# Performance work log

Hardware: AMD Instinct MI355X
Metric: run time of the kernel (lower is better)

## Reference

```python
import jax, jax.numpy as jnp
import numpy as np
from jax import lax

N = 500_000          # num voxels
LATENT = 128         # latent_dim
DESC = 32            # descriptor_dim
G = 128              # voxel grid side
B = 2                # batches
K = 256              # max centers (hardcoded topk in module)
TAU = 0.1
MIN_SCORE = 0.5
R = 1                # peak_radius
BASE = G + 2         # padded hash base so stencil offsets never collide
NEG = -1e30

# radius_graph with r = R + 0.1 on integer coords -> exact stencil offsets
_OFFS = [(dx, dy, dz)
         for dx in range(-R, R + 1)
         for dy in range(-R, R + 1)
         for dz in range(-R, R + 1)
         if dx * dx + dy * dy + dz * dz <= (R + 0.1) ** 2]
DKEYS = np.array([dx * BASE * BASE + dy * BASE + dz for dx, dy, dz in _OFFS], np.int32)  # (7,)


def setup_inputs() -> dict:
    rng = np.random.default_rng(0)
    lin = rng.choice(B * G ** 3, size=N, replace=False)  # unique occupied voxels
    b = lin // G ** 3
    rem = lin % G ** 3
    coords = np.stack([b, rem // (G * G), (rem // G) % G, rem % G], 1).astype(np.int32)
    key = jax.random.key(0)
    k1, k2, k3, k4, k5, k6, k7 = jax.random.split(key, 7)
    s = 1.0 / np.sqrt(LATENT)
    return {
        "coords": jnp.asarray(coords),
        "voxel_feats": jax.random.normal(k1, (N, LATENT), jnp.float32),
        "centroid_scores": jax.random.uniform(k2, (N, 1), jnp.float32),
        "Wv": jax.random.normal(k3, (LATENT, DESC), jnp.float32) * s,
        "bv": jax.random.normal(k4, (DESC,), jnp.float32) * 0.01,
        "Wc": jax.random.normal(k5, (LATENT, DESC), jnp.float32) * s,
        "bc": jax.random.normal(k6, (DESC,), jnp.float32) * 0.01,
        "bg": jax.random.normal(k7, (DESC,), jnp.float32) * 0.02,
    }


def _find_centroid_peaks(coords, voxel_feats, centroid_scores):
    """Replicates _find_centroid_peaks with fixed K=256 padding (torch.no_grad block)."""
    n = coords.shape[0]
    scores = centroid_scores[:, 0]
    mask = scores > TAU
    # hash each voxel; +1 padding so stencil neighbors never wrap across rows/batches
    keyv = (coords[:, 0] * BASE + coords[:, 1] + 1) * BASE * BASE \
         + (coords[:, 2] + 1) * BASE + (coords[:, 3] + 1)
    order = jnp.argsort(keyv)
    keys_s = keyv[order]
    ms = jnp.where(mask, scores, NEG)  # only masked points participate in the graph

    nk = keyv[:, None] + jnp.asarray(DKEYS)[None, :]          # (N,7) neighbor keys
    pos = jnp.clip(jnp.searchsorted(keys_s, nk.ravel()), 0, n - 1).reshape(n, len(DKEYS))
    found = keys_s[pos] == nk                                  # (N,7) geometric hit
    j = order[pos]                                             # (N,7) neighbor index
    found = found & mask[j] & mask[:, None]                    # edges need both masked

    neigh_max = jnp.max(jnp.where(found, ms[j], NEG), axis=1)  # scatter_max over edges
    peak_mask = mask & (scores >= neigh_max - 1e-6) & (scores >= MIN_SCORE)

    # topk-256 peaks (padded with NEG if fewer)
    vals, top_idx = lax.top_k(jnp.where(peak_mask, scores, NEG), K)
    valid_peak = vals > NEG / 2
    owner_init = jnp.full((n,), -1, jnp.int32).at[top_idx].set(
        jnp.where(valid_peak, jnp.arange(K, dtype=jnp.int32), -1))

    # ownership propagation: a voxel is owned by a neighboring (top) peak; self-loop
    # keeps peaks owning themselves. Conflicts resolved by max (torch scatter is
    # nondeterministic here).
    owner = jnp.max(jnp.where(found, owner_init[j], -1), axis=1)
    owner = jnp.where(mask, owner, -1)

    valid = owner >= 0
    owner_safe = jnp.where(valid, owner, 0)
    sums = jax.ops.segment_sum(jnp.where(valid[:, None], voxel_feats, 0.0),
                               owner_safe, num_segments=K)
    counts = jax.ops.segment_sum(valid.astype(jnp.float32), owner_safe, num_segments=K)
    feat_mean = sums / jnp.maximum(counts, 1.0)[:, None]       # scatter_mean
    conf = jnp.where(valid_peak, vals, 0.0)[:, None]           # (K,1)
    return conf, feat_mean


def reference(coords, voxel_feats, centroid_scores, Wv, bv, Wc, bc, bg):
    conf, feat_mean = _find_centroid_peaks(coords, voxel_feats, centroid_scores)
    conf = lax.stop_gradient(conf)
    feat_mean = lax.stop_gradient(feat_mean)
    voxel_desc = voxel_feats @ Wv + bv              # 1x1 sparse conv == linear
    center_desc = feat_mean @ Wc + bc               # 1x1 sparse conv == linear
    cols = jnp.concatenate([bg[None, :], conf * center_desc], axis=0)  # (K+1, DESC)
    instance_output = voxel_desc @ cols.T            # (N, K+1)
    return conf, instance_output
```

## Files before the change

kernel.cpp:

```cpp
#include <hip/hip_runtime.h>
#include <hip/hip_bf16.h>
#include <stdint.h>

#define TAUF 0.1f
#define MIN_SCOREF 0.5f
#define KTOP 256
#define BASE 130
#define BASE2 16900
#define TABLE_N 4394000
#define NEGF (-1e30f)
#define CAP2 3072
#define NS 4096

__global__ void k_build(const int* __restrict__ coords, int* __restrict__ table,
                        int* __restrict__ keys, int n) {
  int i = blockIdx.x * 256 + threadIdx.x;
  if (i >= n) return;
  int4 c = ((const int4*)coords)[i];
  int key = (c.x * BASE + c.y + 1) * BASE2 + (c.z + 1) * BASE + (c.w + 1);
  keys[i] = key;
  table[key] = i;
}

__global__ void k_peak(const float* __restrict__ scores, const int* __restrict__ keys,
                       const int* __restrict__ table, uint2* __restrict__ cand,
                       int* __restrict__ cand_cnt, int n) {
  int i = blockIdx.x * 256 + threadIdx.x;
  if (i >= n) return;
  float s = scores[i];
  if (!(s > TAUF)) return;
  int key = keys[i];
  const int dk[7] = {-BASE2, -BASE, -1, 0, 1, BASE, BASE2};
  float nm = NEGF;
#pragma unroll
  for (int o = 0; o < 7; ++o) {
    int j = table[key + dk[o]];
    if (j >= 0) {
      float sj = scores[j];
      if (sj > TAUF) nm = fmaxf(nm, sj);
    }
  }
  if (s >= nm - 1e-6f && s >= MIN_SCOREF) {
    int p = atomicAdd(cand_cnt, 1);
    if (p < n) cand[p] = make_uint2(__float_as_uint(s), (unsigned)i);
  }
}

__global__ void k_select(const uint2* __restrict__ cand, const int* __restrict__ cand_cnt,
                         float* __restrict__ conf_out, int* __restrict__ owner_init,
                         int* __restrict__ peak_vox) {
  __shared__ int hist[2048];
  __shared__ unsigned long long keys_s[NS];
  __shared__ int bstar_s, m_s;
  int t = threadIdx.x;
  int nc = *cand_cnt;
  for (int b = t; b < 2048; b += 1024) hist[b] = 0;
  if (t == 0) m_s = 0;
  __syncthreads();
  for (int idx = t; idx < nc; idx += 1024) {
    unsigned sb = cand[idx].x;
    int b = (int)((sb - 0x3F000000u) >> 12);
    b = min(max(b, 0), 2047);
    atomicAdd(&hist[b], 1);
  }
  __syncthreads();
  if (t == 0) {
    int target = min(nc, KTOP);
    int run = 0, bs = 0;
    for (int b = 2047; b >= 0; --b) {
      run += hist[b];
      if (run >= target) { bs = b; break; }
    }
    bstar_s = bs;
  }
  __syncthreads();
  int bs = bstar_s;
  for (int idx = t; idx < nc; idx += 1024) {
    uint2 cv = cand[idx];
    int b = (int)((cv.x - 0x3F000000u) >> 12);
    b = min(max(b, 0), 2047);
    if (b >= bs) {
      int p = atomicAdd(&m_s, 1);
      if (p < CAP2)
        keys_s[p] = ((unsigned long long)cv.x << 32) | (unsigned)(~cv.y);
    }
  }
  __syncthreads();
  int m = min(m_s, CAP2);
  for (int idx = t; idx < NS; idx += 1024)
    if (idx >= m) keys_s[idx] = 0ULL;
  __syncthreads();
  for (int k2 = 2; k2 <= NS; k2 <<= 1) {
    for (int j2 = k2 >> 1; j2 > 0; j2 >>= 1) {
      for (int i = t; i < NS; i += 1024) {
        int ixj = i ^ j2;
        if (ixj > i) {
          unsigned long long a = keys_s[i], b = keys_s[ixj];
          bool descSeg = ((i & k2) == 0);
          bool sw = descSeg ? (a < b) : (a > b);
          if (sw) { keys_s[i] = b; keys_s[ixj] = a; }
        }
      }
      __syncthreads();
    }
  }
  if (t < KTOP) {
    int navail = min(nc, KTOP);
    if (t < navail) {
      unsigned long long kk = keys_s[t];
      float sc = __uint_as_float((unsigned)(kk >> 32));
      int vi = (int)(~(unsigned)(kk & 0xFFFFFFFFu));
      conf_out[t] = sc;
      owner_init[vi] = t;
      peak_vox[t] = vi;
    } else {
      conf_out[t] = 0.0f;
      peak_vox[t] = -1;
    }
  }
}

__global__ void k_owner(const float* __restrict__ scores, const int* __restrict__ keys,
                        const int* __restrict__ table, const int* __restrict__ owner_init,
                        const int* __restrict__ peak_vox, int* __restrict__ visited,
                        const float* __restrict__ feats, float* __restrict__ sums,
                        float* __restrict__ counts) {
  int t = blockIdx.x * blockDim.x + threadIdx.x;
  if (t >= KTOP * 7) return;
  int p = t / 7, o = t % 7;
  int v0 = peak_vox[p];
  if (v0 < 0) return;
  const int dk[7] = {-BASE2, -BASE, -1, 0, 1, BASE, BASE2};
  int v = table[keys[v0] + dk[o]];
  if (v < 0) return;
  if (!(scores[v] > TAUF)) return;
  int kv = keys[v];
  int own = -1;
#pragma unroll
  for (int oo = 0; oo < 7; ++oo) {
    int j = table[kv + dk[oo]];
    if (j >= 0 && scores[j] > TAUF) own = max(own, owner_init[j]);
  }
  if (own < 0) return;
  if (atomicCAS(&visited[v], 0, 1) == 0) {
    atomicAdd(&counts[own], 1.0f);
    const float* fv = feats + (size_t)v * 128;
    float* so = sums + own * 128;
    for (int d = 0; d < 128; ++d) atomicAdd(&so[d], fv[d]);
  }
}

__global__ void k_cols(const float* __restrict__ sums, const float* __restrict__ counts,
                       const float* __restrict__ conf, const float* __restrict__ Wc,
                       const float* __restrict__ bc, const float* __restrict__ bg,
                       float* __restrict__ colsT) {
  int gid = blockIdx.x * blockDim.x + threadIdx.x;
  if (gid >= 32 * 257) return;
  int kd = gid / 257, jo = gid % 257;
  float val;
  if (jo == 0) {
    val = bg[kd];
  } else {
    int p = jo - 1;
    float inv = 1.0f / fmaxf(counts[p], 1.0f);
    float acc = bc[kd];
    const float* sp = sums + p * 128;
    for (int c = 0; c < 128; ++c) acc += sp[c] * inv * Wc[c * 32 + kd];
    val = conf[p] * acc;
  }
  colsT[kd * 257 + jo] = val;
}

__global__ __launch_bounds__(256) void k_desc(const float* __restrict__ feats,
                                              const float* __restrict__ Wv,
                                              const float* __restrict__ bv,
                                              float* __restrict__ desc, int n) {
  __shared__ __align__(16) float Wv_s[128 * 32];
  __shared__ float feats_s[64 * 129];
  __shared__ float bv_s[32];
  int t = threadIdx.x;
  int rbase = blockIdx.x * 64;
  {
    const float4* src = (const float4*)Wv;
    float4* dst = (float4*)Wv_s;
    for (int i = t; i < 1024; i += 256) dst[i] = src[i];
  }
  if (t < 32) bv_s[t] = bv[t];
  for (int it = 0; it < 8; ++it) {
    int idx = t + it * 256;
    int r = idx >> 5, c4 = idx & 31;
    int row = rbase + r;
    float4 v = make_float4(0.f, 0.f, 0.f, 0.f);
    if (row < n) v = *(const float4*)(feats + (size_t)row * 128 + c4 * 4);
    float* fd = &feats_s[r * 129 + c4 * 4];
    fd[0] = v.x; fd[1] = v.y; fd[2] = v.z; fd[3] = v.w;
  }
  __syncthreads();
  int r = t & 63;
  int k0 = (t >> 6) * 8;
  float acc[8];
#pragma unroll
  for (int q = 0; q < 8; ++q) acc[q] = bv_s[k0 + q];
  const float* fr = &feats_s[r * 129];
#pragma unroll 8
  for (int c = 0; c < 128; ++c) {
    float f = fr[c];
    float4 w0 = *(const float4*)&Wv_s[c * 32 + k0];
    float4 w1 = *(const float4*)&Wv_s[c * 32 + k0 + 4];
    acc[0] += f * w0.x; acc[1] += f * w0.y; acc[2] += f * w0.z; acc[3] += f * w0.w;
    acc[4] += f * w1.x; acc[5] += f * w1.y; acc[6] += f * w1.z; acc[7] += f * w1.w;
  }
  int row = rbase + r;
  if (row < n) {
    float4* dp = (float4*)(desc + (size_t)row * 32 + k0);
    dp[0] = make_float4(acc[0], acc[1], acc[2], acc[3]);
    dp[1] = make_float4(acc[4], acc[5], acc[6], acc[7]);
  }
}

__global__ __launch_bounds__(256) void k_out(const float* __restrict__ desc,
                                             const float* __restrict__ colsT,
                                             float* __restrict__ out, int n) {
  __shared__ __align__(16) float cols_s[32 * 260];
  __shared__ float desc_s[192 * 33];
  int t = threadIdx.x;
  int rbase = blockIdx.x * 192;
  for (int idx = t; idx < 32 * 257; idx += 256) {
    int kd = idx / 257, jo = idx % 257;
    cols_s[kd * 260 + jo] = colsT[idx];
  }
  for (int it = 0; it < 6; ++it) {
    int idx = t + it * 256;
    int r = idx >> 3, c4 = idx & 7;
    int row = rbase + r;
    float4 v = make_float4(0.f, 0.f, 0.f, 0.f);
    if (row < n) v = *(const float4*)(desc + (size_t)row * 32 + c4 * 4);
    float* dd = &desc_s[r * 33 + c4 * 4];
    dd[0] = v.x; dd[1] = v.y; dd[2] = v.z; dd[3] = v.w;
  }
  __syncthreads();
  int jg = t & 7, rg = t >> 3;
  int r0 = rg * 6;
  for (int jc = 0; jc < 4; ++jc) {
    int j0 = jc * 64 + jg * 8;
    float acc[6][8];
#pragma unroll
    for (int a = 0; a < 6; ++a)
#pragma unroll
      for (int b = 0; b < 8; ++b) acc[a][b] = 0.f;
#pragma unroll 4
    for (int k = 0; k < 32; ++k) {
      float4 c0 = *(const float4*)&cols_s[k * 260 + j0];
      float4 c1 = *(const float4*)&cols_s[k * 260 + j0 + 4];
      float cj[8] = {c0.x, c0.y, c0.z, c0.w, c1.x, c1.y, c1.z, c1.w};
#pragma unroll
      for (int rr = 0; rr < 6; ++rr) {
        float f = desc_s[(r0 + rr) * 33 + k];
#pragma unroll
        for (int jj = 0; jj < 8; ++jj) acc[rr][jj] += f * cj[jj];
      }
    }
#pragma unroll
    for (int rr = 0; rr < 6; ++rr) {
      int row = rbase + r0 + rr;
      if (row < n) {
        float* op = out + 256 + (size_t)row * 257 + j0;
#pragma unroll
        for (int jj = 0; jj < 8; ++jj) op[jj] = acc[rr][jj];
      }
    }
  }
  if (t < 192) {
    float accT = 0.f;
#pragma unroll 8
    for (int k = 0; k < 32; ++k) accT += desc_s[t * 33 + k] * cols_s[k * 260 + 256];
    int row = rbase + t;
    if (row < n) out[256 + (size_t)row * 257 + 256] = accT;
  }
}

__global__ void k_M(const float* __restrict__ Wv, const float* __restrict__ bv,
                    const float* __restrict__ colsT, float* __restrict__ M) {
  int gid = blockIdx.x * 256 + threadIdx.x;
  if (gid >= 129 * 257) return;
  int c = gid / 257, jo = gid % 257;
  const float* wrow = (c < 128) ? (Wv + c * 32) : bv;
  float acc = 0.f;
  for (int k = 0; k < 32; ++k) acc += wrow[k] * colsT[k * 257 + jo];
  M[gid] = acc;
}
__global__ void k_fused(const float* __restrict__ feats, const float* __restrict__ M,
                        float* __restrict__ out, int n) {
  long long gid = (long long)blockIdx.x * 256 + threadIdx.x;
  if (gid >= (long long)n * 257) return;
  int i = (int)(gid / 257), jo = (int)(gid % 257);
  const float* fr = feats + (size_t)i * 128;
  float acc = M[128 * 257 + jo];
  for (int c = 0; c < 128; ++c) acc += fr[c] * M[c * 257 + jo];
  out[256 + gid] = acc;
}

extern "C" void kernel_launch(void* const* d_in, const int* in_sizes, int n_in,
                              void* d_out, int out_size, void* d_ws, size_t ws_size,
                              hipStream_t stream) {
  const int*   coords = (const int*)d_in[0];
  const float* feats  = (const float*)d_in[1];
  const float* scores = (const float*)d_in[2];
  const float* Wv     = (const float*)d_in[3];
  const float* bv     = (const float*)d_in[4];
  const float* Wc     = (const float*)d_in[5];
  const float* bc     = (const float*)d_in[6];
  const float* bg     = (const float*)d_in[7];
  float* out = (float*)d_out;
  int n = in_sizes[0] / 4;

  char* ws = (char*)d_ws;
  size_t off = 0;
  auto alloc = [&](size_t bytes) -> char* {
    char* p = ws + off;
    off = (off + bytes + 255) & ~(size_t)255;
    return p;
  };
  int*   table      = (int*)alloc((size_t)TABLE_N * 4);
  int*   keys       = (int*)alloc((size_t)n * 4);
  int*   owner_init = (int*)alloc((size_t)n * 4);
  char*  zero_base  = ws + off;
  int*   visited    = (int*)alloc((size_t)n * 4);
  int*   cand_cnt   = (int*)alloc(256);
  float* sums       = (float*)alloc(256 * 128 * 4);
  float* counts     = (float*)alloc(256 * 4);
  size_t zero_bytes = (size_t)((ws + off) - zero_base);
  uint2* cand       = (uint2*)alloc((size_t)n * 8);
  int*   peak_vox   = (int*)alloc(KTOP * 4);
  float* colsT      = (float*)alloc(32 * 257 * 4);
  size_t off_common = off;
  float* desc       = (float*)alloc((size_t)n * 32 * 4);
  bool use_split = (off <= ws_size);

  hipMemsetAsync(table, 0xFF, (size_t)TABLE_N * 4, stream);
  hipMemsetAsync(owner_init, 0xFF, (size_t)n * 4, stream);
  hipMemsetAsync(zero_base, 0, zero_bytes, stream);

  int nb = (n + 255) / 256;
  k_build<<<nb, 256, 0, stream>>>(coords, table, keys, n);
  k_peak<<<nb, 256, 0, stream>>>(scores, keys, table, cand, cand_cnt, n);
  k_select<<<1, 1024, 0, stream>>>(cand, cand_cnt, out, owner_init, peak_vox);
  k_owner<<<7, 256, 0, stream>>>(scores, keys, table, owner_init, peak_vox,
                                 visited, feats, sums, counts);
  k_cols<<<(32 * 257 + 255) / 256, 256, 0, stream>>>(sums, counts, out, Wc, bc, bg, colsT);

  if (use_split) {
    k_desc<<<(n + 63) / 64, 256, 0, stream>>>(feats, Wv, bv, desc, n);
    k_out<<<(n + 191) / 192, 256, 0, stream>>>(desc, colsT, out, n);
  } else {
    off = off_common;
    float* M = (float*)alloc(129 * 257 * 4);
    k_M<<<(129 * 257 + 255) / 256, 256, 0, stream>>>(Wv, bv, colsT, M);
    long long total = (long long)n * 257;
    int nbf = (int)((total + 255) / 256);
    k_fused<<<nbf, 256, 0, stream>>>(feats, M, out, n);
  }
}
```

Baseline: 1.194 ms.

## Fuse descriptor and output GEMMs, build histogram in peak kernel, shrink sort

The voxel-descriptor GEMM and the output GEMM are merged into one kernel that processes 192 rows per block in chunks of 32. This removes the round trip of the N×32 descriptor buffer through global memory. The score histogram is now built with global atomics inside the peak kernel, and the selection kernel uses a two-level prefix scan. The bitonic sort is sized to the next power of two at or above the candidate count instead of a fixed 4096. The two memsets are merged into one by placing table and owner_init next to each other. The fused kernel uses more shared memory and has less register reuse per output (one row per thread group instead of six), which may lower GEMM efficiency.

```diff
diff --git a/kernel.cpp b/kernel.cpp
--- a/kernel.cpp
+++ b/kernel.cpp
@@ -1,5 +1,4 @@
 #include <hip/hip_runtime.h>
-#include <hip/hip_bf16.h>
 #include <stdint.h>
 
 #define TAUF 0.1f
@@ -10,7 +9,9 @@
 #define TABLE_N 4394000
 #define NEGF (-1e30f)
 #define CAP2 3072
-#define NS 4096
+#define NSMAX 4096
+#define ROWS_PB 192
+#define CHUNK 32
 
 __global__ void k_build(const int* __restrict__ coords, int* __restrict__ table,
                         int* __restrict__ keys, int n) {
@@ -24,7 +25,7 @@
 
 __global__ void k_peak(const float* __restrict__ scores, const int* __restrict__ keys,
                        const int* __restrict__ table, uint2* __restrict__ cand,
-                       int* __restrict__ cand_cnt, int n) {
+                       int* __restrict__ cand_cnt, int* __restrict__ hist, int n) {
   int i = blockIdx.x * 256 + threadIdx.x;
   if (i >= n) return;
   float s = scores[i];
@@ -43,33 +44,51 @@
   if (s >= nm - 1e-6f && s >= MIN_SCOREF) {
     int p = atomicAdd(cand_cnt, 1);
     if (p < n) cand[p] = make_uint2(__float_as_uint(s), (unsigned)i);
-  }
-}
-
-__global__ void k_select(const uint2* __restrict__ cand, const int* __restrict__ cand_cnt,
-                         float* __restrict__ conf_out, int* __restrict__ owner_init,
-                         int* __restrict__ peak_vox) {
-  __shared__ int hist[2048];
-  __shared__ unsigned long long keys_s[NS];
+    unsigned sb = __float_as_uint(s);
+    int b = (int)((sb - 0x3F000000u) >> 12);
+    b = min(max(b, 0), 2047);
+    atomicAdd(&hist[b], 1);
+  }
+}
+
+__global__ __launch_bounds__(1024) void k_select(const uint2* __restrict__ cand,
+                                                 const int* __restrict__ cand_cnt,
+                                                 const int* __restrict__ hist,
+                                                 float* __restrict__ conf_out,
+                                                 int* __restrict__ owner_init,
+                                                 int* __restrict__ peak_vox) {
+  __shared__ int hist_s[2048];
+  __shared__ int part[64];
+  __shared__ unsigned long long keys_s[NSMAX];
   __shared__ int bstar_s, m_s;
   int t = threadIdx.x;
   int nc = *cand_cnt;
-  for (int b = t; b < 2048; b += 1024) hist[b] = 0;
+  for (int b = t; b < 2048; b += 1024) hist_s[b] = hist[b];
   if (t == 0) m_s = 0;
   __syncthreads();
-  for (int idx = t; idx < nc; idx += 1024) {
-    unsigned sb = cand[idx].x;
-    int b = (int)((sb - 0x3F000000u) >> 12);
-    b = min(max(b, 0), 2047);
-    atomicAdd(&hist[b], 1);
+  if (t < 64) {
+    int acc = 0;
+    for (int b = t * 32; b < t * 32 + 32; ++b) acc += hist_s[b];
+    part[t] = acc;
   }
   __syncthreads();
   if (t == 0) {
     int target = min(nc, KTOP);
-    int run = 0, bs = 0;
-    for (int b = 2047; b >= 0; --b) {
-      run += hist[b];
-      if (run >= target) { bs = b; break; }
+    int bs = 0;
+    if (target > 0) {
+      int run = 0, w = 63;
+      for (; w >= 0; --w) {
+        if (run + part[w] >= target) break;
+        run += part[w];
+      }
+      if (w < 0) {
+        bs = 0;
+      } else {
+        for (int b = w * 32 + 31;; --b) {
+          run += hist_s[b];
+          if (run >= target || b == w * 32) { bs = b; break; }
+        }
+      }
     }
     bstar_s = bs;
   }
@@ -87,12 +106,14 @@
   }
   __syncthreads();
   int m = min(m_s, CAP2);
-  for (int idx = t; idx < NS; idx += 1024)
+  int ns = 256;
+  while (ns < m) ns <<= 1;
+  for (int idx = t; idx < ns; idx += 1024)
     if (idx >= m) keys_s[idx] = 0ULL;
   __syncthreads();
-  for (int k2 = 2; k2 <= NS; k2 <<= 1) {
+  for (int k2 = 2; k2 <= ns; k2 <<= 1) {
     for (int j2 = k2 >> 1; j2 > 0; j2 >>= 1) {
-      for (int i = t; i < NS; i += 1024) {
+      for (int i = t; i < ns; i += 1024) {
         int ixj = i ^ j2;
         if (ixj > i) {
           unsigned long long a = keys_s[i], b = keys_s[ixj];
@@ -171,133 +192,90 @@
   colsT[kd * 257 + jo] = val;
 }
 
-__global__ __launch_bounds__(256) void k_desc(const float* __restrict__ feats,
-                                              const float* __restrict__ Wv,
-                                              const float* __restrict__ bv,
-                                              float* __restrict__ desc, int n) {
+__global__ __launch_bounds__(256) void k_go(const float* __restrict__ feats,
+                                            const float* __restrict__ Wv,
+                                            const float* __restrict__ bv,
+                                            const float* __restrict__ colsT,
+                                            float* __restrict__ out, int n) {
   __shared__ __align__(16) float Wv_s[128 * 32];
-  __shared__ float feats_s[64 * 129];
+  __shared__ __align__(16) float cols_s[32 * 260];
+  __shared__ __align__(16) float feats_s[CHUNK * 129];
+  __shared__ float desc_s[CHUNK * 33];
   __shared__ float bv_s[32];
   int t = threadIdx.x;
-  int rbase = blockIdx.x * 64;
+  int rbase = blockIdx.x * ROWS_PB;
   {
     const float4* src = (const float4*)Wv;
     float4* dst = (float4*)Wv_s;
     for (int i = t; i < 1024; i += 256) dst[i] = src[i];
   }
-  if (t < 32) bv_s[t] = bv[t];
-  for (int it = 0; it < 8; ++it) {
-    int idx = t + it * 256;
-    int r = idx >> 5, c4 = idx & 31;
-    int row = rbase + r;
-    float4 v = make_float4(0.f, 0.f, 0.f, 0.f);
-    if (row < n) v = *(const float4*)(feats + (size_t)row * 128 + c4 * 4);
-    float* fd = &feats_s[r * 129 + c4 * 4];
-    fd[0] = v.x; fd[1] = v.y; fd[2] = v.z; fd[3] = v.w;
-  }
-  __syncthreads();
-  int r = t & 63;
-  int k0 = (t >> 6) * 8;
-  float acc[8];
-#pragma unroll
-  for (int q = 0; q < 8; ++q) acc[q] = bv_s[k0 + q];
-  const float* fr = &feats_s[r * 129];
-#pragma unroll 8
-  for (int c = 0; c < 128; ++c) {
-    float f = fr[c];
-    float4 w0 = *(const float4*)&Wv_s[c * 32 + k0];
-    float4 w1 = *(const float4*)&Wv_s[c * 32 + k0 + 4];
-    acc[0] += f * w0.x; acc[1] += f * w0.y; acc[2] += f * w0.z; acc[3] += f * w0.w;
-    acc[4] += f * w1.x; acc[5] += f * w1.y; acc[6] += f * w1.z; acc[7] += f * w1.w;
-  }
-  int row = rbase + r;
-  if (row < n) {
-    float4* dp = (float4*)(desc + (size_t)row * 32 + k0);
-    dp[0] = make_float4(acc[0], acc[1], acc[2], acc[3]);
-    dp[1] = make_float4(acc[4], acc[5], acc[6], acc[7]);
-  }
-}
-
-__global__ __launch_bounds__(256) void k_out(const float* __restrict__ desc,
-                                             const float* __restrict__ colsT,
-                                             float* __restrict__ out, int n) {
-  __shared__ __align__(16) float cols_s[32 * 260];
-  __shared__ float desc_s[192 * 33];
-  int t = threadIdx.x;
-  int rbase = blockIdx.x * 192;
   for (int idx = t; idx < 32 * 257; idx += 256) {
     int kd = idx / 257, jo = idx % 257;
     cols_s[kd * 260 + jo] = colsT[idx];
   }
-  for (int it = 0; it < 6; ++it) {
-    int idx = t + it * 256;
-    int r = idx >> 3, c4 = idx & 7;
-    int row = rbase + r;
-    float4 v = make_float4(0.f, 0.f, 0.f, 0.f);
-    if (row < n) v = *(const float4*)(desc + (size_t)row * 32 + c4 * 4);
-    float* dd = &desc_s[r * 33 + c4 * 4];
-    dd[0] = v.x; dd[1] = v.y; dd[2] = v.z; dd[3] = v.w;
-  }
-  __syncthreads();
-  int jg = t & 7, rg = t >> 3;
-  int r0 = rg * 6;
-  for (int jc = 0; jc < 4; ++jc) {
-    int j0 = jc * 64 + jg * 8;
-    float acc[6][8];
-#pragma unroll
-    for (int a = 0; a < 6; ++a)
-#pragma unroll
-      for (int b = 0; b < 8; ++b) acc[a][b] = 0.f;
+  if (t < 32) bv_s[t] = bv[t];
+
+  for (int c0 = 0; c0 < ROWS_PB; c0 += CHUNK) {
+    __syncthreads();
+    {
+      int idx = t;
+      for (int it = 0; it < 4; ++it, idx += 256) {
+        int r = idx >> 5, q = idx & 31;
+        int row = rbase + c0 + r;
+        float4 v = make_float4(0.f, 0.f, 0.f, 0.f);
+        if (row < n) v = *(const float4*)(feats + (size_t)row * 128 + q * 4);
+        float* fd = &feats_s[r * 129 + q * 4];
+        fd[0] = v.x; fd[1] = v.y; fd[2] = v.z; fd[3] = v.w;
+      }
+    }
+    __syncthreads();
+    {
+      int r = t & 31, k0 = (t >> 5) * 4;
+      float a0 = bv_s[k0], a1 = bv_s[k0 + 1], a2 = bv_s[k0 + 2], a3 = bv_s[k0 + 3];
+      const float* fr = &feats_s[r * 129];
+#pragma unroll 8
+      for (int c = 0; c < 128; ++c) {
+        float f = fr[c];
+        float4 w = *(const float4*)&Wv_s[c * 32 + k0];
+        a0 += f * w.x; a1 += f * w.y; a2 += f * w.z; a3 += f * w.w;
+      }
+      float* dd = &desc_s[r * 33 + k0];
+      dd[0] = a0; dd[1] = a1; dd[2] = a2; dd[3] = a3;
+    }
+    __syncthreads();
+    {
+      int rg = t >> 3, jg = t & 7;
+      int row = rbase + c0 + rg;
+      if (row < n) {
+        float dreg[32];
+#pragma unroll
+        for (int k = 0; k < 32; ++k) dreg[k] = desc_s[rg * 33 + k];
+        float* op = out + 256 + (size_t)row * 257;
+        for (int jc = 0; jc < 4; ++jc) {
+          int j0 = jc * 64 + jg * 8;
+          float acc[8];
+#pragma unroll
+          for (int j = 0; j < 8; ++j) acc[j] = 0.f;
 #pragma unroll 4
-    for (int k = 0; k < 32; ++k) {
-      float4 c0 = *(const float4*)&cols_s[k * 260 + j0];
-      float4 c1 = *(const float4*)&cols_s[k * 260 + j0 + 4];
-      float cj[8] = {c0.x, c0.y, c0.z, c0.w, c1.x, c1.y, c1.z, c1.w};
-#pragma unroll
-      for (int rr = 0; rr < 6; ++rr) {
-        float f = desc_s[(r0 + rr) * 33 + k];
-#pragma unroll
-        for (int jj = 0; jj < 8; ++jj) acc[rr][jj] += f * cj[jj];
-      }
-    }
-#pragma unroll
-    for (int rr = 0; rr < 6; ++rr) {
-      int row = rbase + r0 + rr;
-      if (row < n) {
-        float* op = out + 256 + (size_t)row * 257 + j0;
-#pragma unroll
-        for (int jj = 0; jj < 8; ++jj) op[jj] = acc[rr][jj];
-      }
-    }
-  }
-  if (t < 192) {
-    float accT = 0.f;
+          for (int k = 0; k < 32; ++k) {
+            float f = dreg[k];
+            float4 cA = *(const float4*)&cols_s[k * 260 + j0];
+            float4 cB = *(const float4*)&cols_s[k * 260 + j0 + 4];
+            acc[0] += f * cA.x; acc[1] += f * cA.y; acc[2] += f * cA.z; acc[3] += f * cA.w;
+            acc[4] += f * cB.x; acc[5] += f * cB.y; acc[6] += f * cB.z; acc[7] += f * cB.w;
+          }
+#pragma unroll
+          for (int j = 0; j < 8; ++j) op[j0 + j] = acc[j];
+        }
+        if (jg == 0) {
+          float accT = 0.f;
 #pragma unroll 8
-    for (int k = 0; k < 32; ++k) accT += desc_s[t * 33 + k] * cols_s[k * 260 + 256];
-    int row = rbase + t;
-    if (row < n) out[256 + (size_t)row * 257 + 256] = accT;
-  }
-}
-
-__global__ void k_M(const float* __restrict__ Wv, const float* __restrict__ bv,
-                    const float* __restrict__ colsT, float* __restrict__ M) {
-  int gid = blockIdx.x * 256 + threadIdx.x;
-  if (gid >= 129 * 257) return;
-  int c = gid / 257, jo = gid % 257;
-  const float* wrow = (c < 128) ? (Wv + c * 32) : bv;
-  float acc = 0.f;
-  for (int k = 0; k < 32; ++k) acc += wrow[k] * colsT[k * 257 + jo];
-  M[gid] = acc;
-}
-__global__ void k_fused(const float* __restrict__ feats, const float* __restrict__ M,
-                        float* __restrict__ out, int n) {
-  long long gid = (long long)blockIdx.x * 256 + threadIdx.x;
-  if (gid >= (long long)n * 257) return;
-  int i = (int)(gid / 257), jo = (int)(gid % 257);
-  const float* fr = feats + (size_t)i * 128;
-  float acc = M[128 * 257 + jo];
-  for (int c = 0; c < 128; ++c) acc += fr[c] * M[c * 257 + jo];
-  out[256 + gid] = acc;
+          for (int k = 0; k < 32; ++k) accT += dreg[k] * cols_s[k * 260 + 256];
+          op[256] = accT;
+        }
+      }
+    }
+  }
 }
 
 extern "C" void kernel_launch(void* const* d_in, const int* in_sizes, int n_in,
@@ -322,42 +300,30 @@
     return p;
   };
   int*   table      = (int*)alloc((size_t)TABLE_N * 4);
+  int*   owner_init = (int*)alloc((size_t)n * 4);
+  size_t ff_bytes   = off;
   int*   keys       = (int*)alloc((size_t)n * 4);
-  int*   owner_init = (int*)alloc((size_t)n * 4);
   char*  zero_base  = ws + off;
   int*   visited    = (int*)alloc((size_t)n * 4);
   int*   cand_cnt   = (int*)alloc(256);
+  int*   hist       = (int*)alloc(2048 * 4);
   float* sums       = (float*)alloc(256 * 128 * 4);
   float* counts     = (float*)alloc(256 * 4);
   size_t zero_bytes = (size_t)((ws + off) - zero_base);
   uint2* cand       = (uint2*)alloc((size_t)n * 8);
   int*   peak_vox   = (int*)alloc(KTOP * 4);
   float* colsT      = (float*)alloc(32 * 257 * 4);
-  size_t off_common = off;
-  float* desc       = (float*)alloc((size_t)n * 32 * 4);
-  bool use_split = (off <= ws_size);
-
-  hipMemsetAsync(table, 0xFF, (size_t)TABLE_N * 4, stream);
-  hipMemsetAsync(owner_init, 0xFF, (size_t)n * 4, stream);
+  (void)ws_size;
+
+  hipMemsetAsync(table, 0xFF, ff_bytes, stream);
   hipMemsetAsync(zero_base, 0, zero_bytes, stream);
 
   int nb = (n + 255) / 256;
   k_build<<<nb, 256, 0, stream>>>(coords, table, keys, n);
-  k_peak<<<nb, 256, 0, stream>>>(scores, keys, table, cand, cand_cnt, n);
-  k_select<<<1, 1024, 0, stream>>>(cand, cand_cnt, out, owner_init, peak_vox);
+  k_peak<<<nb, 256, 0, stream>>>(scores, keys, table, cand, cand_cnt, hist, n);
+  k_select<<<1, 1024, 0, stream>>>(cand, cand_cnt, hist, out, owner_init, peak_vox);
   k_owner<<<7, 256, 0, stream>>>(scores, keys, table, owner_init, peak_vox,
                                  visited, feats, sums, counts);
   k_cols<<<(32 * 257 + 255) / 256, 256, 0, stream>>>(sums, counts, out, Wc, bc, bg, colsT);
-
-  if (use_split) {
-    k_desc<<<(n + 63) / 64, 256, 0, stream>>>(feats, Wv, bv, desc, n);
-    k_out<<<(n + 191) / 192, 256, 0, stream>>>(desc, colsT, out, n);
-  } else {
-    off = off_common;
-    float* M = (float*)alloc(129 * 257 * 4);
-    k_M<<<(129 * 257 + 255) / 256, 256, 0, stream>>>(Wv, bv, colsT, M);
-    long long total = (long long)n * 257;
-    int nbf = (int)((total + 255) / 256);
-    k_fused<<<nbf, 256, 0, stream>>>(feats, M, out, n);
-  }
-}
+  k_go<<<(n + ROWS_PB - 1) / ROWS_PB, 256, 0, stream>>>(feats, Wv, bv, colsT, out, n);
+}
```

Measured after the change: 1.174 ms. Within noise of the previous version (-1.6%).
